# Kernel tuning notes

Measured on AMD Instinct MI355X. Metric: run time of the kernel, lower is better.

## Reference

```python
import jax, jax.numpy as jnp
import numpy as np
import math

D = 512; H = 8; NL = 6; VOCAB = 256; NC = 10; L = 1024; B = 4
DK = D // H
SCALE = math.sqrt(DK)
EMB_SCALE = math.sqrt(D)
EPS = 1e-5


def _pos_encoding(seq_len, d_model):
    pos = jnp.arange(seq_len, dtype=jnp.float32)[:, None]
    div = jnp.exp(-jnp.arange(0, d_model, 2, dtype=jnp.float32) / d_model * math.log(10000.0))
    pe = jnp.zeros((seq_len, d_model), dtype=jnp.float32)
    pe = pe.at[:, 0::2].set(jnp.sin(pos * div))
    pe = pe.at[:, 1::2].set(jnp.cos(pos * div))
    return pe


def _layer_norm(x, g, b):
    m = jnp.mean(x, axis=-1, keepdims=True)
    v = jnp.mean(jnp.square(x - m), axis=-1, keepdims=True)
    return (x - m) * jax.lax.rsqrt(v + EPS) * g + b


def setup_inputs() -> dict:
    key = jax.random.key(0)
    ks = jax.random.split(key, 18)
    s = 0.02  # keep activations in a sane range so softmax is not saturated
    return {
        "tokens": jax.random.randint(ks[0], (B, L), 0, VOCAB, dtype=jnp.int32),
        "emb_table": jax.random.normal(ks[1], (VOCAB, D), jnp.float32) * s,
        "Wq": jax.random.normal(ks[2], (NL, D, D), jnp.float32) * s,
        "bq": jax.random.normal(ks[3], (NL, D), jnp.float32) * s,
        "Wkv": jax.random.normal(ks[4], (NL, 2 * D, D), jnp.float32) * s,
        "bkv": jax.random.normal(ks[5], (NL, 2 * D), jnp.float32) * s,
        "Wo": jax.random.normal(ks[6], (NL, D, D), jnp.float32) * s,
        "bo": jax.random.normal(ks[7], (NL, D), jnp.float32) * s,
        "ln1_g": jnp.ones((NL, D), jnp.float32),
        "ln1_b": jnp.zeros((NL, D), jnp.float32),
        "W1": jax.random.normal(ks[8], (NL, 4 * D, D), jnp.float32) * s,
        "b1": jax.random.normal(ks[9], (NL, 4 * D), jnp.float32) * s,
        "W2": jax.random.normal(ks[10], (NL, D, 4 * D), jnp.float32) * s,
        "b2": jax.random.normal(ks[11], (NL, D), jnp.float32) * s,
        "ln2_g": jnp.ones((NL, D), jnp.float32),
        "ln2_b": jnp.zeros((NL, D), jnp.float32),
        "Wc": jax.random.normal(ks[12], (NC, D), jnp.float32) * s,
        "bc": jax.random.normal(ks[13], (NC,), jnp.float32) * s,
    }


def reference(tokens, emb_table, Wq, bq, Wkv, bkv, Wo, bo, ln1_g, ln1_b,
              W1, b1, W2, b2, ln2_g, ln2_b, Wc, bc):
    seq_len = tokens.shape[1]
    pe = _pos_encoding(seq_len, D)  # [L, D]
    x = emb_table[tokens] * EMB_SCALE + pe[None]  # [B, L, D]  (dropout = identity in eval)

    def block(x, p):
        wq, bq_, wkv, bkv_, wo, bo_, g1, be1, w1, bb1, w2, bb2, g2, be2 = p
        h = _layer_norm(x, g1, be1)
        q = h @ wq.T + bq_                       # [B, L, D]
        kv = h @ wkv.T + bkv_                    # [B, L, 2D]
        k, v = kv[..., :D], kv[..., D:]
        # split heads: [B, H, L, dk]
        q = q.reshape(*q.shape[:2], H, DK).transpose(0, 2, 1, 3)
        k = k.reshape(*k.shape[:2], H, DK).transpose(0, 2, 1, 3)
        v = v.reshape(*v.shape[:2], H, DK).transpose(0, 2, 1, 3)
        score = jnp.einsum('bhqd,bhkd->bhqk', q, k) / SCALE  # [B, H, L, L]
        attn = jax.nn.softmax(score, axis=-1)
        av = jnp.einsum('bhqk,bhkd->bhqd', attn, v)
        av = av.transpose(0, 2, 1, 3).reshape(*x.shape)      # merge heads
        x = x + (av @ wo.T + bo_)
        h2 = _layer_norm(x, g2, be2)
        ffn = jax.nn.relu(h2 @ w1.T + bb1) @ w2.T + bb2
        x = x + ffn
        return x, None

    params = (Wq, bq, Wkv, bkv, Wo, bo, ln1_g, ln1_b, W1, b1, W2, b2, ln2_g, ln2_b)
    x, _ = jax.lax.scan(block, x, params)
    return x @ Wc.T + bc  # [B, L, NC]
```

## Files before the change

kernel.cpp:

```cpp
#include <hip/hip_runtime.h>
#include <math.h>

#define D 512
#define HEADS 8
#define NLAYER 6
#define LSEQ 1024
#define BATCH 4
#define DKH 64
#define MTOK (BATCH*LSEQ)
#define EPS 1e-5f
#define EMB_SCALE 22.627416997969522f
#define INV_SCALE 0.125f

typedef __attribute__((ext_vector_type(8))) __bf16 bf16x8;
typedef __attribute__((ext_vector_type(4))) float f32x4;

__device__ __forceinline__ unsigned short f2bf(float x) {
    union { float f; unsigned u; } v; v.f = x;
    unsigned r = (v.u + 0x7FFFu + ((v.u >> 16) & 1u)) >> 16;
    return (unsigned short)r;
}
__device__ __forceinline__ unsigned pack2(float a, float b) {
    return (unsigned)f2bf(a) | ((unsigned)f2bf(b) << 16);
}
__device__ __forceinline__ void gl_lds16(const unsigned short* g, unsigned short* l) {
    __builtin_amdgcn_global_load_lds(
        (const __attribute__((address_space(1))) unsigned*)g,
        (__attribute__((address_space(3))) unsigned*)l, 16, 0, 0);
}

__global__ __launch_bounds__(128) void embed_kernel(
    const int* __restrict__ tokens, const float* __restrict__ emb,
    float* __restrict__ x)
{
    int row = blockIdx.x;
    int pos = row & (LSEQ - 1);
    int tok = tokens[row];
    int c = threadIdx.x * 4;
    float4 e = *(const float4*)(emb + (size_t)tok * D + c);
    float o[4] = {e.x, e.y, e.z, e.w};
#pragma unroll
    for (int i = 0; i < 4; ++i) {
        int col = c + i;
        int ii = col & ~1;
        float dv = expf(-(float)ii * (9.210340371976184f / (float)D));
        float a = (float)pos * dv;
        float pe = (col & 1) ? cosf(a) : sinf(a);
        o[i] = o[i] * EMB_SCALE + pe;
    }
    float4 r; r.x = o[0]; r.y = o[1]; r.z = o[2]; r.w = o[3];
    *(float4*)(x + (size_t)row * D + c) = r;
}

__global__ __launch_bounds__(256) void ln_kernel(
    const float* __restrict__ x, const float* __restrict__ g,
    const float* __restrict__ b, unsigned short* __restrict__ h)
{
    int lane = threadIdx.x & 63;
    int row = blockIdx.x * 4 + (threadIdx.x >> 6);
    const float* xr = x + (size_t)row * D + lane * 8;
    float4 v0 = *(const float4*)(xr);
    float4 v1 = *(const float4*)(xr + 4);
    float s = v0.x + v0.y + v0.z + v0.w + v1.x + v1.y + v1.z + v1.w;
#pragma unroll
    for (int off = 32; off; off >>= 1) s += __shfl_xor(s, off, 64);
    float m = s * (1.0f / D);
    float d0 = v0.x - m, d1 = v0.y - m, d2 = v0.z - m, d3 = v0.w - m;
    float d4 = v1.x - m, d5 = v1.y - m, d6 = v1.z - m, d7 = v1.w - m;
    float ss = d0*d0 + d1*d1 + d2*d2 + d3*d3 + d4*d4 + d5*d5 + d6*d6 + d7*d7;
#pragma unroll
    for (int off = 32; off; off >>= 1) ss += __shfl_xor(ss, off, 64);
    float inv = rsqrtf(ss * (1.0f / D) + EPS);
    const float* gp = g + lane * 8;
    const float* bp = b + lane * 8;
    float4 g0 = *(const float4*)(gp), g1 = *(const float4*)(gp + 4);
    float4 b0 = *(const float4*)(bp), b1 = *(const float4*)(bp + 4);
    uint4 o;
    o.x = pack2(d0 * inv * g0.x + b0.x, d1 * inv * g0.y + b0.y);
    o.y = pack2(d2 * inv * g0.z + b0.z, d3 * inv * g0.w + b0.w);
    o.z = pack2(d4 * inv * g1.x + b1.x, d5 * inv * g1.y + b1.y);
    o.w = pack2(d6 * inv * g1.z + b1.z, d7 * inv * g1.w + b1.w);
    *(uint4*)(h + (size_t)row * D + lane * 8) = o;
}

__global__ __launch_bounds__(256) void wconv_kernel(
    const float* __restrict__ Wq, const float* __restrict__ Wkv,
    const float* __restrict__ Wo, const float* __restrict__ W1,
    const float* __restrict__ W2, const float* __restrict__ bq,
    const float* __restrict__ bkv, unsigned short* __restrict__ dst,
    float* __restrict__ bias_out)
{
    if (blockIdx.x == 1536) {
        for (int i = threadIdx.x; i < 1536; i += 256)
            bias_out[i] = (i < 512) ? bq[i] : bkv[i - 512];
        return;
    }
    int gid = blockIdx.x * 256 + threadIdx.x;
    int e = gid * 8;
    const float* src;
    if      (e < 262144)  src = Wq  + e;
    else if (e < 786432)  src = Wkv + (e - 262144);
    else if (e < 1048576) src = Wo  + (e - 786432);
    else if (e < 2097152) src = W1  + (e - 1048576);
    else                  src = W2  + (e - 2097152);
    float4 a = *(const float4*)src;
    float4 b = *(const float4*)(src + 4);
    uint4 o;
    o.x = pack2(a.x, a.y); o.y = pack2(a.z, a.w);
    o.z = pack2(b.x, b.y); o.w = pack2(b.z, b.w);
    *(uint4*)(dst + e) = o;
}

template<int OMODE, int BM>
__global__ __launch_bounds__(256) void gemm_bf16(
    const unsigned short* __restrict__ A, const unsigned short* __restrict__ W,
    const float* __restrict__ bias, const float* __restrict__ X,
    void* __restrict__ C, void* __restrict__ C2, void* __restrict__ C3,
    int M, int N, int K)
{
    constexpr int WM = BM / 64;
    constexpr int WN = 4 / WM;
    constexpr int NI = 8 / WN;
    __shared__ __align__(16) unsigned short As[2][BM * 64];
    __shared__ __align__(16) unsigned short Bs[2][128 * 64];
    const int tid = threadIdx.x;
    const int wave = tid >> 6, lane = tid & 63;
    const int quad = lane >> 4, l16 = lane & 15;
    const int wm = wave / WN, wn = wave % WN;
    const int bm = blockIdx.y * BM, bn = blockIdx.x * 128;

    const int rS  = tid >> 3;
    const int csw = (((tid & 7) ^ (rS & 7)) << 3);
    const unsigned short* Asrc = A + (size_t)(bm + rS) * K + csw;
    const unsigned short* Bsrc = W + (size_t)(bn + rS) * K + csw;

    f32x4 acc[4][NI];
#pragma unroll
    for (int mi = 0; mi < 4; ++mi)
#pragma unroll
        for (int ni = 0; ni < NI; ++ni) acc[mi][ni] = (f32x4){0.f, 0.f, 0.f, 0.f};

    const int nt = K >> 6;

#pragma unroll
    for (int i = 0; i < BM / 32; ++i)
        gl_lds16(Asrc + (size_t)(i * 32) * K, &As[0][i * 2048 + tid * 8]);
#pragma unroll
    for (int i = 0; i < 4; ++i)
        gl_lds16(Bsrc + (size_t)(i * 32) * K, &Bs[0][i * 2048 + tid * 8]);
    __syncthreads();

    for (int t = 0; t < nt; ++t) {
        const int cur = t & 1;
        if (t + 1 < nt) {
            const int k0 = (t + 1) << 6;
#pragma unroll
            for (int i = 0; i < BM / 32; ++i)
                gl_lds16(Asrc + (size_t)(i * 32) * K + k0, &As[cur ^ 1][i * 2048 + tid * 8]);
#pragma unroll
            for (int i = 0; i < 4; ++i)
                gl_lds16(Bsrc + (size_t)(i * 32) * K + k0, &Bs[cur ^ 1][i * 2048 + tid * 8]);
        }
#pragma unroll
        for (int kc = 0; kc < 2; ++kc) {
            const int gch = (kc << 2) | quad;
            bf16x8 af[4], bfr[NI];
#pragma unroll
            for (int mi = 0; mi < 4; ++mi) {
                const int ra = wm * 64 + mi * 16 + l16;
                af[mi] = *(const bf16x8*)&As[cur][ra * 64 + ((gch ^ (ra & 7)) << 3)];
            }
#pragma unroll
            for (int ni = 0; ni < NI; ++ni) {
                const int rb = wn * (128 / WN) + ni * 16 + l16;
                bfr[ni] = *(const bf16x8*)&Bs[cur][rb * 64 + ((gch ^ (rb & 7)) << 3)];
            }
#pragma unroll
            for (int mi = 0; mi < 4; ++mi)
#pragma unroll
                for (int ni = 0; ni < NI; ++ni)
                    acc[mi][ni] = __builtin_amdgcn_mfma_f32_16x16x32_bf16(
                        af[mi], bfr[ni], acc[mi][ni], 0, 0, 0);
        }
        __syncthreads();
    }

    const int er = bm + wm * 64;
    const int ec = bn + wn * (128 / WN);

    if (OMODE == 0) {
        float* Cf = (float*)C;
#pragma unroll
        for (int ni = 0; ni < NI; ++ni) {
            int c = ec + ni * 16 + l16;
            float bv = bias[c];
#pragma unroll
            for (int mi = 0; mi < 4; ++mi)
#pragma unroll
                for (int r = 0; r < 4; ++r) {
                    int m = er + mi * 16 + quad * 4 + r;
                    Cf[(size_t)m * N + c] = acc[mi][ni][r] + bv + X[(size_t)m * N + c];
                }
        }
    } else if (OMODE == 1) {
        unsigned short* Cb = (unsigned short*)C;
#pragma unroll
        for (int ni = 0; ni < NI; ++ni) {
            int c = ec + ni * 16 + l16;
            float bv = bias[c];
#pragma unroll
            for (int mi = 0; mi < 4; ++mi)
#pragma unroll
                for (int r = 0; r < 4; ++r) {
                    int m = er + mi * 16 + quad * 4 + r;
                    Cb[(size_t)m * N + c] = f2bf(fmaxf(acc[mi][ni][r] + bv, 0.f));
                }
        }
    } else {
        if (bn < 512) {
            unsigned short* Qp = (unsigned short*)C;
#pragma unroll
            for (int ni = 0; ni < NI; ++ni) {
                int c = ec + ni * 16 + l16;
                float bv = bias[c];
                int hh = c >> 6, dd = c & 63;
                size_t cbase = (size_t)(dd >> 5) * 512 + (size_t)((dd >> 3) & 3) * 128 + (dd & 7);
#pragma unroll
                for (int mi = 0; mi < 4; ++mi)
#pragma unroll
                    for (int r = 0; r < 4; ++r) {
                        int m = er + mi * 16 + quad * 4 + r;
                        int b = m >> 10, t = m & 1023;
                        Qp[(size_t)(b * 8 + hh) * 65536 + (size_t)(t >> 4) * 1024
                           + cbase + (size_t)(t & 15) * 8] =
                            f2bf((acc[mi][ni][r] + bv) * INV_SCALE);
                    }
            }
        } else if (bn < 1024) {
            unsigned short* Kp = (unsigned short*)C2;
#pragma unroll
            for (int ni = 0; ni < NI; ++ni) {
                int c = ec + ni * 16 + l16;
                float bv = bias[c];
                int c2 = c - 512;
                int hh = c2 >> 6, dd = c2 & 63;
                size_t cbase = (size_t)(dd >> 5) * 512 + (size_t)((dd >> 3) & 3) * 128 + (dd & 7);
#pragma unroll
                for (int mi = 0; mi < 4; ++mi)
#pragma unroll
                    for (int r = 0; r < 4; ++r) {
                        int m = er + mi * 16 + quad * 4 + r;
                        int b = m >> 10, t = m & 1023;
                        Kp[(size_t)(b * 8 + hh) * 65536 + (size_t)(t >> 4) * 1024
                           + cbase + (size_t)(t & 15) * 8] =
                            f2bf(acc[mi][ni][r] + bv);
                    }
            }
        } else {
            unsigned short* Vp = (unsigned short*)C3;
#pragma unroll
            for (int ni = 0; ni < NI; ++ni) {
                int c = ec + ni * 16 + l16;
                float bv = bias[c];
                int c2 = c - 1024;
                int hh = c2 >> 6, dd = c2 & 63;
                size_t dbase = (size_t)(dd >> 4) * 16384 + (size_t)(dd & 15) * 8;
#pragma unroll
                for (int mi = 0; mi < 4; ++mi) {
                    int t0 = er + mi * 16 + quad * 4;
                    int b = t0 >> 10, tt = t0 & 1023;
                    ushort4 o;
                    o.x = f2bf(acc[mi][ni][0] + bv);
                    o.y = f2bf(acc[mi][ni][1] + bv);
                    o.z = f2bf(acc[mi][ni][2] + bv);
                    o.w = f2bf(acc[mi][ni][3] + bv);
                    *(ushort4*)(Vp + (size_t)(b * 8 + hh) * 65536 + dbase
                                + (size_t)(tt >> 5) * 512
                                + (size_t)((tt >> 3) & 3) * 128 + (tt & 7)) = o;
                }
            }
        }
    }
}

__global__ __launch_bounds__(256, 2) void attn_mfma(
    const unsigned short* __restrict__ Qb, const unsigned short* __restrict__ Kb,
    const unsigned short* __restrict__ Vt, unsigned short* __restrict__ av)
{
    __shared__ __align__(16) unsigned short Ks[2][4096];
    __shared__ __align__(16) unsigned short Vs[2][4096];
    const int tid = threadIdx.x;
    const int wave = tid >> 6, lane = tid & 63;
    const int quad = lane >> 4, l16 = lane & 15;
    const int bh = blockIdx.x & 31;
    const int b = bh >> 3, h = bh & 7;
    const int q0 = (blockIdx.x >> 5) * 64 + wave * 16;

    const unsigned short* qp   = Qb + (size_t)bh * 65536 + (size_t)(q0 >> 4) * 1024 + lane * 8;
    const unsigned short* ksrc = Kb + (size_t)bh * 65536;
    const unsigned short* vsrc = Vt + (size_t)bh * 65536;

    const int sA  = ((((2 * quad) & 3) << 4) + l16) << 2;
    const int sB2 = ((((2 * quad + 1) & 3) << 4) + l16) << 2;

    bf16x8 qf0 = *(const bf16x8*)qp;
    bf16x8 qf1 = *(const bf16x8*)(qp + 512);

    f32x4 o[4];
#pragma unroll
    for (int nf = 0; nf < 4; ++nf) o[nf] = (f32x4){0.f, 0.f, 0.f, 0.f};
    float lp = 0.f;

    auto STAGE = [&](int j, int buf) {
        gl_lds16(ksrc + (size_t)j * 64 + tid * 8,        &Ks[buf][tid * 8]);
        gl_lds16(ksrc + (size_t)j * 64 + 2048 + tid * 8, &Ks[buf][2048 + tid * 8]);
        gl_lds16(vsrc + (size_t)j * 16 + (size_t)(wave >> 1) * 16384
                      + (wave & 1) * 512 + lane * 8,
                 &Vs[buf][wave * 512 + lane * 8]);
        gl_lds16(vsrc + (size_t)j * 16 + (size_t)((wave + 4) >> 1) * 16384
                      + ((wave + 4) & 1) * 512 + lane * 8,
                 &Vs[buf][2048 + wave * 512 + lane * 8]);
    };

    STAGE(0, 0);
    __syncthreads();

    for (int it = 0; it < 16; ++it) {
        const int cur = it & 1;
        if (it + 1 < 16) STAGE((it + 1) * 64, cur ^ 1);
        unsigned pk01[4], pk23[4];
#pragma unroll
        for (int nf = 0; nf < 4; ++nf) {
            bf16x8 kc0 = *(const bf16x8*)&Ks[cur][nf * 1024 + lane * 8];
            bf16x8 kc1 = *(const bf16x8*)&Ks[cur][nf * 1024 + 512 + lane * 8];
            f32x4 z = {0.f, 0.f, 0.f, 0.f};
            z = __builtin_amdgcn_mfma_f32_16x16x32_bf16(kc0, qf0, z, 0, 0, 0);
            z = __builtin_amdgcn_mfma_f32_16x16x32_bf16(kc1, qf1, z, 0, 0, 0);
            float p0 = __expf(z[0]);
            float p1 = __expf(z[1]);
            float p2 = __expf(z[2]);
            float p3 = __expf(z[3]);
            lp += (p0 + p1) + (p2 + p3);
            pk01[nf] = pack2(p0, p1);
            pk23[nf] = pack2(p2, p3);
        }
        union PU { unsigned d[4]; bf16x8 v; } f0, f1;
        {
            unsigned a0, a1;
            a0 = (unsigned)__builtin_amdgcn_ds_bpermute(sA,  (int)pk01[0]);
            a1 = (unsigned)__builtin_amdgcn_ds_bpermute(sA,  (int)pk01[1]);
            f0.d[0] = (quad < 2) ? a0 : a1;
            a0 = (unsigned)__builtin_amdgcn_ds_bpermute(sA,  (int)pk23[0]);
            a1 = (unsigned)__builtin_amdgcn_ds_bpermute(sA,  (int)pk23[1]);
            f0.d[1] = (quad < 2) ? a0 : a1;
            a0 = (unsigned)__builtin_amdgcn_ds_bpermute(sB2, (int)pk01[0]);
            a1 = (unsigned)__builtin_amdgcn_ds_bpermute(sB2, (int)pk01[1]);
            f0.d[2] = (quad < 2) ? a0 : a1;
            a0 = (unsigned)__builtin_amdgcn_ds_bpermute(sB2, (int)pk23[0]);
            a1 = (unsigned)__builtin_amdgcn_ds_bpermute(sB2, (int)pk23[1]);
            f0.d[3] = (quad < 2) ? a0 : a1;
            a0 = (unsigned)__builtin_amdgcn_ds_bpermute(sA,  (int)pk01[2]);
            a1 = (unsigned)__builtin_amdgcn_ds_bpermute(sA,  (int)pk01[3]);
            f1.d[0] = (quad < 2) ? a0 : a1;
            a0 = (unsigned)__builtin_amdgcn_ds_bpermute(sA,  (int)pk23[2]);
            a1 = (unsigned)__builtin_amdgcn_ds_bpermute(sA,  (int)pk23[3]);
            f1.d[1] = (quad < 2) ? a0 : a1;
            a0 = (unsigned)__builtin_amdgcn_ds_bpermute(sB2, (int)pk01[2]);
            a1 = (unsigned)__builtin_amdgcn_ds_bpermute(sB2, (int)pk01[3]);
            f1.d[2] = (quad < 2) ? a0 : a1;
            a0 = (unsigned)__builtin_amdgcn_ds_bpermute(sB2, (int)pk23[2]);
            a1 = (unsigned)__builtin_amdgcn_ds_bpermute(sB2, (int)pk23[3]);
            f1.d[3] = (quad < 2) ? a0 : a1;
        }
#pragma unroll
        for (int nf = 0; nf < 4; ++nf) {
            bf16x8 vf0 = *(const bf16x8*)&Vs[cur][nf * 1024 + lane * 8];
            bf16x8 vf1 = *(const bf16x8*)&Vs[cur][nf * 1024 + 512 + lane * 8];
            o[nf] = __builtin_amdgcn_mfma_f32_16x16x32_bf16(f0.v, vf0, o[nf], 0, 0, 0);
            o[nf] = __builtin_amdgcn_mfma_f32_16x16x32_bf16(f1.v, vf1, o[nf], 0, 0, 0);
        }
        __syncthreads();
    }

    float ts = lp;
    ts += __shfl_xor(ts, 16, 64);
    ts += __shfl_xor(ts, 32, 64);
    union { float f; int i; } tsb; tsb.f = ts;
#pragma unroll
    for (int r = 0; r < 4; ++r) {
        union { int i; float f; } dv;
        dv.i = __builtin_amdgcn_ds_bpermute((quad * 20 + r) << 2, tsb.i);
        float inv = 1.0f / dv.f;
        int q = q0 + quad * 4 + r;
#pragma unroll
        for (int nf = 0; nf < 4; ++nf)
            av[((size_t)(b * 1024 + q)) * D + h * 64 + nf * 16 + l16] =
                f2bf(o[nf][r] * inv);
    }
}

__global__ __launch_bounds__(256) void cls_kernel(
    const float* __restrict__ x, const float* __restrict__ Wc,
    const float* __restrict__ bc, float* __restrict__ out)
{
    int lane = threadIdx.x & 63;
    int row = blockIdx.x * 4 + (threadIdx.x >> 6);
    const float* xr = x + (size_t)row * D + lane * 8;
    float4 v0 = *(const float4*)xr;
    float4 v1 = *(const float4*)(xr + 4);
    float acc[10];
#pragma unroll
    for (int c = 0; c < 10; ++c) {
        const float* wr = Wc + c * D + lane * 8;
        float4 w0 = *(const float4*)wr;
        float4 w1 = *(const float4*)(wr + 4);
        acc[c] = v0.x*w0.x + v0.y*w0.y + v0.z*w0.z + v0.w*w0.w
               + v1.x*w1.x + v1.y*w1.y + v1.z*w1.z + v1.w*w1.w;
    }
#pragma unroll
    for (int c = 0; c < 10; ++c)
#pragma unroll
        for (int off = 32; off; off >>= 1) acc[c] += __shfl_xor(acc[c], off, 64);
    if (lane == 0) {
#pragma unroll
        for (int c = 0; c < 10; ++c) out[(size_t)row * 10 + c] = acc[c] + bc[c];
    }
}

extern "C" void kernel_launch(void* const* d_in, const int* in_sizes, int n_in,
                              void* d_out, int out_size, void* d_ws, size_t ws_size,
                              hipStream_t stream)
{
    const int*   tokens = (const int*)  d_in[0];
    const float* emb    = (const float*)d_in[1];
    const float* Wq     = (const float*)d_in[2];
    const float* bq     = (const float*)d_in[3];
    const float* Wkv    = (const float*)d_in[4];
    const float* bkv    = (const float*)d_in[5];
    const float* Wo     = (const float*)d_in[6];
    const float* bo     = (const float*)d_in[7];
    const float* ln1g   = (const float*)d_in[8];
    const float* ln1b   = (const float*)d_in[9];
    const float* W1     = (const float*)d_in[10];
    const float* b1     = (const float*)d_in[11];
    const float* W2     = (const float*)d_in[12];
    const float* b2     = (const float*)d_in[13];
    const float* ln2g   = (const float*)d_in[14];
    const float* ln2b   = (const float*)d_in[15];
    const float* Wc     = (const float*)d_in[16];
    const float* bc     = (const float*)d_in[17];
    float* out = (float*)d_out;

    float* x  = (float*)d_ws;
    unsigned short* hb  = (unsigned short*)(x + (size_t)MTOK * D);
    unsigned short* Qb  = hb  + (size_t)MTOK * D;
    unsigned short* Kb  = Qb  + (size_t)32 * 1024 * 64;
    unsigned short* Vt  = Kb  + (size_t)32 * 1024 * 64;
    unsigned short* avb = Vt  + (size_t)32 * 1024 * 64;
    unsigned short* f1b = Qb;
    unsigned short* wl  = avb + (size_t)32 * 1024 * 64;
    float* wbias = (float*)(wl + (size_t)3145728);

    const size_t oWo = 786432, oW1 = 1048576, oW2 = 2097152;

    embed_kernel<<<MTOK, 128, 0, stream>>>(tokens, emb, x);

    for (int l = 0; l < NLAYER; ++l) {
        wconv_kernel<<<1537, 256, 0, stream>>>(
            Wq  + (size_t)l * 262144,  Wkv + (size_t)l * 524288,
            Wo  + (size_t)l * 262144,  W1  + (size_t)l * 1048576,
            W2  + (size_t)l * 1048576, bq + (size_t)l * 512,
            bkv + (size_t)l * 1024, wl, wbias);
        ln_kernel<<<MTOK / 4, 256, 0, stream>>>(x, ln1g + l * D, ln1b + l * D, hb);
        gemm_bf16<2,128><<<dim3(12, 32), 256, 0, stream>>>(
            hb, wl, wbias, nullptr, Qb, Kb, Vt, MTOK, 1536, 512);
        attn_mfma<<<512, 256, 0, stream>>>(Qb, Kb, Vt, avb);
        gemm_bf16<0,64><<<dim3(4, 64), 256, 0, stream>>>(
            avb, wl + oWo, bo + l * D, x, x, nullptr, nullptr, MTOK, D, D);
        ln_kernel<<<MTOK / 4, 256, 0, stream>>>(x, ln2g + l * D, ln2b + l * D, hb);
        gemm_bf16<1,128><<<dim3(16, 32), 256, 0, stream>>>(
            hb, wl + oW1, b1 + l * 4 * D, nullptr, f1b, nullptr, nullptr, MTOK, 4 * D, D);
        gemm_bf16<0,64><<<dim3(4, 64), 256, 0, stream>>>(
            f1b, wl + oW2, b2 + l * D, x, x, nullptr, nullptr, MTOK, D, 4 * D);
    }

    cls_kernel<<<MTOK / 4, 256, 0, stream>>>(x, Wc, bc, out);
}
```

Before: 815.5 us.

## Convert all layer weights upfront in one prep kernel and retune GEMM tiles

```diff
diff --git a/kernel.cpp b/kernel.cpp
--- a/kernel.cpp
+++ b/kernel.cpp
@@ -29,27 +29,54 @@
         (__attribute__((address_space(3))) unsigned*)l, 16, 0, 0);
 }
 
-__global__ __launch_bounds__(128) void embed_kernel(
+__global__ __launch_bounds__(256) void prep_kernel(
     const int* __restrict__ tokens, const float* __restrict__ emb,
-    float* __restrict__ x)
-{
-    int row = blockIdx.x;
-    int pos = row & (LSEQ - 1);
-    int tok = tokens[row];
-    int c = threadIdx.x * 4;
-    float4 e = *(const float4*)(emb + (size_t)tok * D + c);
-    float o[4] = {e.x, e.y, e.z, e.w};
-#pragma unroll
-    for (int i = 0; i < 4; ++i) {
-        int col = c + i;
-        int ii = col & ~1;
-        float dv = expf(-(float)ii * (9.210340371976184f / (float)D));
-        float a = (float)pos * dv;
-        float pe = (col & 1) ? cosf(a) : sinf(a);
-        o[i] = o[i] * EMB_SCALE + pe;
-    }
-    float4 r; r.x = o[0]; r.y = o[1]; r.z = o[2]; r.w = o[3];
-    *(float4*)(x + (size_t)row * D + c) = r;
+    const float* __restrict__ Wq, const float* __restrict__ Wkv,
+    const float* __restrict__ Wo, const float* __restrict__ W1,
+    const float* __restrict__ W2, const float* __restrict__ bq,
+    const float* __restrict__ bkv, unsigned short* __restrict__ wl,
+    float* __restrict__ wbias, float* __restrict__ x)
+{
+    const int bid = blockIdx.x;
+    if (bid < 9216) {
+        const int l = bid / 1536;
+        const int e = (bid - l * 1536) * 2048 + threadIdx.x * 8;
+        const float* src;
+        if      (e < 262144)  src = Wq  + (size_t)l * 262144  + e;
+        else if (e < 786432)  src = Wkv + (size_t)l * 524288  + (e - 262144);
+        else if (e < 1048576) src = Wo  + (size_t)l * 262144  + (e - 786432);
+        else if (e < 2097152) src = W1  + (size_t)l * 1048576 + (e - 1048576);
+        else                  src = W2  + (size_t)l * 1048576 + (e - 2097152);
+        float4 a = *(const float4*)src;
+        float4 b = *(const float4*)(src + 4);
+        uint4 o;
+        o.x = pack2(a.x, a.y); o.y = pack2(a.z, a.w);
+        o.z = pack2(b.x, b.y); o.w = pack2(b.z, b.w);
+        *(uint4*)(wl + (size_t)l * 3145728 + e) = o;
+    } else if (bid == 9216) {
+        for (int i = threadIdx.x; i < 9216; i += 256) {
+            int l = i / 1536, j = i - l * 1536;
+            wbias[i] = (j < 512) ? bq[l * 512 + j] : bkv[l * 1024 + (j - 512)];
+        }
+    } else {
+        int row = (bid - 9217) * 2 + (threadIdx.x >> 7);
+        int pos = row & (LSEQ - 1);
+        int tok = tokens[row];
+        int c = (threadIdx.x & 127) * 4;
+        float4 e = *(const float4*)(emb + (size_t)tok * D + c);
+        float o[4] = {e.x, e.y, e.z, e.w};
+#pragma unroll
+        for (int i = 0; i < 4; ++i) {
+            int col = c + i;
+            int ii = col & ~1;
+            float dv = expf(-(float)ii * (9.210340371976184f / (float)D));
+            float a = (float)pos * dv;
+            float pe = (col & 1) ? cosf(a) : sinf(a);
+            o[i] = o[i] * EMB_SCALE + pe;
+        }
+        float4 r; r.x = o[0]; r.y = o[1]; r.z = o[2]; r.w = o[3];
+        *(float4*)(x + (size_t)row * D + c) = r;
+    }
 }
 
 __global__ __launch_bounds__(256) void ln_kernel(
@@ -83,35 +110,7 @@
     *(uint4*)(h + (size_t)row * D + lane * 8) = o;
 }
 
-__global__ __launch_bounds__(256) void wconv_kernel(
-    const float* __restrict__ Wq, const float* __restrict__ Wkv,
-    const float* __restrict__ Wo, const float* __restrict__ W1,
-    const float* __restrict__ W2, const float* __restrict__ bq,
-    const float* __restrict__ bkv, unsigned short* __restrict__ dst,
-    float* __restrict__ bias_out)
-{
-    if (blockIdx.x == 1536) {
-        for (int i = threadIdx.x; i < 1536; i += 256)
-            bias_out[i] = (i < 512) ? bq[i] : bkv[i - 512];
-        return;
-    }
-    int gid = blockIdx.x * 256 + threadIdx.x;
-    int e = gid * 8;
-    const float* src;
-    if      (e < 262144)  src = Wq  + e;
-    else if (e < 786432)  src = Wkv + (e - 262144);
-    else if (e < 1048576) src = Wo  + (e - 786432);
-    else if (e < 2097152) src = W1  + (e - 1048576);
-    else                  src = W2  + (e - 2097152);
-    float4 a = *(const float4*)src;
-    float4 b = *(const float4*)(src + 4);
-    uint4 o;
-    o.x = pack2(a.x, a.y); o.y = pack2(a.z, a.w);
-    o.z = pack2(b.x, b.y); o.w = pack2(b.z, b.w);
-    *(uint4*)(dst + e) = o;
-}
-
-template<int OMODE, int BM>
+template<int OMODE, int BM, int BN, int BK>
 __global__ __launch_bounds__(256) void gemm_bf16(
     const unsigned short* __restrict__ A, const unsigned short* __restrict__ W,
     const float* __restrict__ bias, const float* __restrict__ X,
@@ -120,17 +119,20 @@
 {
     constexpr int WM = BM / 64;
     constexpr int WN = 4 / WM;
-    constexpr int NI = 8 / WN;
-    __shared__ __align__(16) unsigned short As[2][BM * 64];
-    __shared__ __align__(16) unsigned short Bs[2][128 * 64];
+    constexpr int NI = BN / (WN * 16);
+    constexpr int CPB = BK / 8;
+    constexpr int RPP = 2048 / BK;
+    __shared__ __align__(16) unsigned short As[2][BM * BK];
+    __shared__ __align__(16) unsigned short Bs[2][BN * BK];
     const int tid = threadIdx.x;
     const int wave = tid >> 6, lane = tid & 63;
     const int quad = lane >> 4, l16 = lane & 15;
     const int wm = wave / WN, wn = wave % WN;
-    const int bm = blockIdx.y * BM, bn = blockIdx.x * 128;
-
-    const int rS  = tid >> 3;
-    const int csw = (((tid & 7) ^ (rS & 7)) << 3);
+    const int bm = blockIdx.y * BM, bn = blockIdx.x * BN;
+
+    const int rS  = tid / CPB;
+    const int ch  = tid % CPB;
+    const int csw = ((ch ^ (rS & 7)) << 3);
     const unsigned short* Asrc = A + (size_t)(bm + rS) * K + csw;
     const unsigned short* Bsrc = W + (size_t)(bn + rS) * K + csw;
 
@@ -140,40 +142,40 @@
 #pragma unroll
         for (int ni = 0; ni < NI; ++ni) acc[mi][ni] = (f32x4){0.f, 0.f, 0.f, 0.f};
 
-    const int nt = K >> 6;
-
-#pragma unroll
-    for (int i = 0; i < BM / 32; ++i)
-        gl_lds16(Asrc + (size_t)(i * 32) * K, &As[0][i * 2048 + tid * 8]);
-#pragma unroll
-    for (int i = 0; i < 4; ++i)
-        gl_lds16(Bsrc + (size_t)(i * 32) * K, &Bs[0][i * 2048 + tid * 8]);
+    const int nt = K / BK;
+
+#pragma unroll
+    for (int i = 0; i < BM / RPP; ++i)
+        gl_lds16(Asrc + (size_t)(i * RPP) * K, &As[0][i * 2048 + tid * 8]);
+#pragma unroll
+    for (int i = 0; i < BN / RPP; ++i)
+        gl_lds16(Bsrc + (size_t)(i * RPP) * K, &Bs[0][i * 2048 + tid * 8]);
     __syncthreads();
 
     for (int t = 0; t < nt; ++t) {
         const int cur = t & 1;
         if (t + 1 < nt) {
-            const int k0 = (t + 1) << 6;
-#pragma unroll
-            for (int i = 0; i < BM / 32; ++i)
-                gl_lds16(Asrc + (size_t)(i * 32) * K + k0, &As[cur ^ 1][i * 2048 + tid * 8]);
-#pragma unroll
-            for (int i = 0; i < 4; ++i)
-                gl_lds16(Bsrc + (size_t)(i * 32) * K + k0, &Bs[cur ^ 1][i * 2048 + tid * 8]);
-        }
-#pragma unroll
-        for (int kc = 0; kc < 2; ++kc) {
+            const int k0 = (t + 1) * BK;
+#pragma unroll
+            for (int i = 0; i < BM / RPP; ++i)
+                gl_lds16(Asrc + (size_t)(i * RPP) * K + k0, &As[cur ^ 1][i * 2048 + tid * 8]);
+#pragma unroll
+            for (int i = 0; i < BN / RPP; ++i)
+                gl_lds16(Bsrc + (size_t)(i * RPP) * K + k0, &Bs[cur ^ 1][i * 2048 + tid * 8]);
+        }
+#pragma unroll
+        for (int kc = 0; kc < BK / 32; ++kc) {
             const int gch = (kc << 2) | quad;
             bf16x8 af[4], bfr[NI];
 #pragma unroll
             for (int mi = 0; mi < 4; ++mi) {
                 const int ra = wm * 64 + mi * 16 + l16;
-                af[mi] = *(const bf16x8*)&As[cur][ra * 64 + ((gch ^ (ra & 7)) << 3)];
+                af[mi] = *(const bf16x8*)&As[cur][ra * BK + ((gch ^ (ra & 7)) << 3)];
             }
 #pragma unroll
             for (int ni = 0; ni < NI; ++ni) {
-                const int rb = wn * (128 / WN) + ni * 16 + l16;
-                bfr[ni] = *(const bf16x8*)&Bs[cur][rb * 64 + ((gch ^ (rb & 7)) << 3)];
+                const int rb = wn * (BN / WN) + ni * 16 + l16;
+                bfr[ni] = *(const bf16x8*)&Bs[cur][rb * BK + ((gch ^ (rb & 7)) << 3)];
             }
 #pragma unroll
             for (int mi = 0; mi < 4; ++mi)
@@ -186,7 +188,7 @@
     }
 
     const int er = bm + wm * 64;
-    const int ec = bn + wn * (128 / WN);
+    const int ec = bn + wn * (BN / WN);
 
     if (OMODE == 0) {
         float* Cf = (float*)C;
@@ -459,29 +461,26 @@
     unsigned short* avb = Vt  + (size_t)32 * 1024 * 64;
     unsigned short* f1b = Qb;
     unsigned short* wl  = avb + (size_t)32 * 1024 * 64;
-    float* wbias = (float*)(wl + (size_t)3145728);
-
-    const size_t oWo = 786432, oW1 = 1048576, oW2 = 2097152;
-
-    embed_kernel<<<MTOK, 128, 0, stream>>>(tokens, emb, x);
+    float* wbias = (float*)(wl + (size_t)6 * 3145728);
+
+    const size_t oWo = 786432, oW1 = 1048576, oW2 = 2097152, LW = 3145728;
+
+    prep_kernel<<<11265, 256, 0, stream>>>(
+        tokens, emb, Wq, Wkv, Wo, W1, W2, bq, bkv, wl, wbias, x);
 
     for (int l = 0; l < NLAYER; ++l) {
-        wconv_kernel<<<1537, 256, 0, stream>>>(
-            Wq  + (size_t)l * 262144,  Wkv + (size_t)l * 524288,
-            Wo  + (size_t)l * 262144,  W1  + (size_t)l * 1048576,
-            W2  + (size_t)l * 1048576, bq + (size_t)l * 512,
-            bkv + (size_t)l * 1024, wl, wbias);
+        const unsigned short* wll = wl + (size_t)l * LW;
         ln_kernel<<<MTOK / 4, 256, 0, stream>>>(x, ln1g + l * D, ln1b + l * D, hb);
-        gemm_bf16<2,128><<<dim3(12, 32), 256, 0, stream>>>(
-            hb, wl, wbias, nullptr, Qb, Kb, Vt, MTOK, 1536, 512);
+        gemm_bf16<2,128,64,64><<<dim3(24, 32), 256, 0, stream>>>(
+            hb, wll, wbias + l * 1536, nullptr, Qb, Kb, Vt, MTOK, 1536, 512);
         attn_mfma<<<512, 256, 0, stream>>>(Qb, Kb, Vt, avb);
-        gemm_bf16<0,64><<<dim3(4, 64), 256, 0, stream>>>(
-            avb, wl + oWo, bo + l * D, x, x, nullptr, nullptr, MTOK, D, D);
+        gemm_bf16<0,64,64,128><<<dim3(8, 64), 256, 0, stream>>>(
+            avb, wll + oWo, bo + l * D, x, x, nullptr, nullptr, MTOK, D, D);
         ln_kernel<<<MTOK / 4, 256, 0, stream>>>(x, ln2g + l * D, ln2b + l * D, hb);
-        gemm_bf16<1,128><<<dim3(16, 32), 256, 0, stream>>>(
-            hb, wl + oW1, b1 + l * 4 * D, nullptr, f1b, nullptr, nullptr, MTOK, 4 * D, D);
-        gemm_bf16<0,64><<<dim3(4, 64), 256, 0, stream>>>(
-            f1b, wl + oW2, b2 + l * D, x, x, nullptr, nullptr, MTOK, D, 4 * D);
+        gemm_bf16<1,128,128,64><<<dim3(16, 32), 256, 0, stream>>>(
+            hb, wll + oW1, b1 + l * 4 * D, nullptr, f1b, nullptr, nullptr, MTOK, 4 * D, D);
+        gemm_bf16<0,64,64,128><<<dim3(8, 64), 256, 0, stream>>>(
+            f1b, wll + oW2, b2 + l * D, x, x, nullptr, nullptr, MTOK, D, 4 * D);
     }
 
     cls_kernel<<<MTOK / 4, 256, 0, stream>>>(x, Wc, bc, out);
```

Result: faster. 687.6 us (-15.7%).
